# Performance work log

Hardware: AMD Instinct MI355X
Metric: run time of the kernel (lower is better)

Reference implementation:

```python
import jax, jax.numpy as jnp
import numpy as np

NUM_HEADS = 16
N_QUBITS = 8  # both attention d_k and FFN qubit count
LN_EPS = 1e-5


def setup_inputs() -> dict:
    key = jax.random.key(0)
    ks = jax.random.split(key, 8)
    B, S, E, F = 8, 4096, 128, 2048
    return {
        "x": jax.random.normal(ks[0], (B, S, E), dtype=jnp.float32),
        "theta_attn": jax.random.normal(ks[1], (N_QUBITS,), dtype=jnp.float32),
        "phi_ffn": jax.random.normal(ks[2], (N_QUBITS,), dtype=jnp.float32),
        "w1": jax.random.normal(ks[3], (F, N_QUBITS), dtype=jnp.float32) * (1.0 / np.sqrt(N_QUBITS)),
        "b1": jax.random.normal(ks[4], (F,), dtype=jnp.float32) * 0.01,
        "w2": jax.random.normal(ks[5], (E, F), dtype=jnp.float32) * (1.0 / np.sqrt(F)),
        "b2": jax.random.normal(ks[6], (E,), dtype=jnp.float32) * 0.01,
        "gamma1": jnp.ones((E,), dtype=jnp.float32),
        "beta1": jnp.zeros((E,), dtype=jnp.float32),
        "gamma2": jnp.ones((E,), dtype=jnp.float32),
        "beta2": jnp.zeros((E,), dtype=jnp.float32),
    }


def _layernorm(y, g, b):
    m = jnp.mean(y, axis=-1, keepdims=True)
    v = jnp.var(y, axis=-1, keepdims=True)
    return (y - m) * jax.lax.rsqrt(v + LN_EPS) * g + b


def _quantum_attn(x, theta):
    # RX(x_k)RX(theta_k) per wire -> per-wire <Z>=cos(x_k+theta_k); CNOT chain + ring
    # maps Z_j -> Z_0..Z_j (j>=1) and Z_0 -> Z_0..Z_{n-1} (Heisenberg picture),
    # so outputs are cumulative products of cosines within each head.
    B, S, E = x.shape
    a = x.reshape(B, S, NUM_HEADS, N_QUBITS) + theta  # (B,S,H,8)
    cp = jnp.cumprod(jnp.cos(a), axis=-1)
    out = jnp.concatenate([cp[..., -1:], cp[..., 1:]], axis=-1)  # wire0 gets full product
    return out.reshape(B, S, E)


def _quantum_ffn(x, phi):
    # RY(phi_j)RX(x_j)|0> -> <Z_j> = cos(phi_j)*cos(x_j); encoder only reads first N_QUBITS feats
    return jnp.cos(phi) * jnp.cos(x[..., :N_QUBITS])  # (B,S,8)


def reference(x, theta_attn, phi_ffn, w1, b1, w2, b2, gamma1, beta1, gamma2, beta2):
    attn = _quantum_attn(x, theta_attn)
    x1 = _layernorm(x + attn, gamma1, beta1)  # dropout is identity in eval
    q = _quantum_ffn(x1, phi_ffn)
    h = jax.nn.relu(jnp.einsum('bsq,fq->bsf', q, w1) + b1)
    ffn = jnp.einsum('bsf,ef->bse', h, w2) + b2
    return _layernorm(x1 + ffn, gamma2, beta2)
```

## Files before the change

### kernel.cpp

```cpp
#include <hip/hip_runtime.h>
#include <hip/hip_bf16.h>

typedef __attribute__((ext_vector_type(8))) short short8;
typedef __attribute__((ext_vector_type(4))) float f32x4;
typedef __attribute__((ext_vector_type(4))) int int4v;

#define LN_EPS 1e-5f

__device__ __forceinline__ unsigned short bf16rn(float f) {
    unsigned int u = __builtin_bit_cast(unsigned int, f);
    u = u + 0x7fffu + ((u >> 16) & 1u);
    return (unsigned short)(u >> 16);
}

__device__ __forceinline__ unsigned cvt_pk(float lo, float hi) {
    unsigned r;
    asm("v_cvt_pk_bf16_f32 %0, %1, %2" : "=v"(r) : "v"(lo), "v"(hi));
    return r;
}

__global__ __launch_bounds__(256) void k_pre(const float* __restrict__ x,
                                             const float* __restrict__ theta,
                                             const float* __restrict__ phi,
                                             const float* __restrict__ gamma1,
                                             const float* __restrict__ beta1,
                                             const float* __restrict__ w1,
                                             const float* __restrict__ b1,
                                             const float* __restrict__ w2,
                                             float* __restrict__ x1,
                                             unsigned short* __restrict__ qpad,
                                             unsigned short* __restrict__ w2b,
                                             unsigned short* __restrict__ w1p) {
    const int tid = threadIdx.x;
    const int bid = blockIdx.x;

    if (bid >= 2048) {
        const int pid = bid - 2048;
        if (pid < 256) {
            int i = (pid * 256 + tid) * 4;
            float4 v = *(const float4*)(w2 + i);
            ushort4 r;
            r.x = bf16rn(v.x); r.y = bf16rn(v.y); r.z = bf16rn(v.z); r.w = bf16rn(v.w);
            *(ushort4*)(w2b + i) = r;
        } else {
            int f = (pid - 256) * 256 + tid;
            float4 wa = *(const float4*)(w1 + (size_t)f * 8);
            float4 wb = *(const float4*)(w1 + (size_t)f * 8 + 4);
            short8 r0, r1;
            r0[0] = (short)bf16rn(wa.x); r0[1] = (short)bf16rn(wa.y);
            r0[2] = (short)bf16rn(wa.z); r0[3] = (short)bf16rn(wa.w);
            r0[4] = (short)bf16rn(wb.x); r0[5] = (short)bf16rn(wb.y);
            r0[6] = (short)bf16rn(wb.z); r0[7] = (short)bf16rn(wb.w);
            r1 = short8{0, 0, 0, 0, 0, 0, 0, 0};
            r1[0] = (short)bf16rn(b1[f]);
            short8 z = short8{0, 0, 0, 0, 0, 0, 0, 0};
            unsigned short* row = w1p + (size_t)f * 32;
            *(short8*)(row) = r0;
            *(short8*)(row + 8) = r1;
            *(short8*)(row + 16) = z;
            *(short8*)(row + 24) = z;
        }
        return;
    }

    const int g = tid >> 4, li = tid & 15;
    const int tok = bid * 16 + g;

    const float* xr = x + (size_t)tok * 128 + li * 8;
    float4 va = *(const float4*)xr;
    float4 vb = *(const float4*)(xr + 4);
    float v[8] = {va.x, va.y, va.z, va.w, vb.x, vb.y, vb.z, vb.w};

    float c[8];
#pragma unroll
    for (int k = 0; k < 8; ++k) c[k] = __cosf(v[k] + theta[k]);
    float cp[8];
    cp[0] = c[0];
#pragma unroll
    for (int k = 1; k < 8; ++k) cp[k] = cp[k - 1] * c[k];

    float y[8];
    y[0] = v[0] + cp[7];
#pragma unroll
    for (int k = 1; k < 8; ++k) y[k] = v[k] + cp[k];

    float s1 = 0.f, s2 = 0.f;
#pragma unroll
    for (int k = 0; k < 8; ++k) { s1 += y[k]; s2 += y[k] * y[k]; }
#pragma unroll
    for (int m = 1; m < 16; m <<= 1) {
        s1 += __shfl_xor(s1, m);
        s2 += __shfl_xor(s2, m);
    }
    float mean = s1 * (1.f / 128.f);
    float var = s2 * (1.f / 128.f) - mean * mean;
    float rs = rsqrtf(var + LN_EPS);

    float4 ga = *(const float4*)(gamma1 + li * 8);
    float4 gb = *(const float4*)(gamma1 + li * 8 + 4);
    float4 ba = *(const float4*)(beta1 + li * 8);
    float4 bb = *(const float4*)(beta1 + li * 8 + 4);
    float gam[8] = {ga.x, ga.y, ga.z, ga.w, gb.x, gb.y, gb.z, gb.w};
    float bet[8] = {ba.x, ba.y, ba.z, ba.w, bb.x, bb.y, bb.z, bb.w};

    float o[8];
#pragma unroll
    for (int k = 0; k < 8; ++k) o[k] = (y[k] - mean) * rs * gam[k] + bet[k];

    float* x1r = x1 + (size_t)tok * 128 + li * 8;
    *(float4*)x1r = make_float4(o[0], o[1], o[2], o[3]);
    *(float4*)(x1r + 4) = make_float4(o[4], o[5], o[6], o[7]);

    if (li == 0) {
        short8 qr;
#pragma unroll
        for (int k = 0; k < 8; ++k)
            qr[k] = (short)bf16rn(__cosf(phi[k]) * __cosf(o[k]));
        *(short8*)(qpad + (size_t)tok * 32) = qr;
    } else if (li < 4) {
        short8 z = short8{0, 0, 0, 0, 0, 0, 0, 0};
        if (li == 1) z[0] = (short)0x3F80;
        *(short8*)(qpad + (size_t)tok * 32 + li * 8) = z;
    }
}

__global__ __launch_bounds__(512, 4) void k_ffn(const float* __restrict__ x1,
                                                const unsigned short* __restrict__ qpad,
                                                const unsigned short* __restrict__ w2b,
                                                const unsigned short* __restrict__ w1p,
                                                const float* __restrict__ b2,
                                                const float* __restrict__ g2,
                                                const float* __restrict__ be2,
                                                float* __restrict__ out) {
    const int tid = threadIdx.x;
    const int wv = tid >> 6;
    const int kh = wv >> 2;
    const int sub = wv & 3;
    const int nh = sub & 1;
    const int mw = sub >> 1;
    const int lane = tid & 63;
    const int li = lane & 15;
    const int lg = lane >> 4;
    const int Tb = blockIdx.x * 64;
    const int lt0 = mw * 32;
    const int t0 = Tb + lt0;

    __shared__ __align__(16) char smem[65536 + 1024];
    unsigned short* Bs = (unsigned short*)smem;
    float (*red)[132] = (float(*)[132])smem;
    float (*sums)[4] = (float(*)[4])(smem + 65536);

    short8 qf[2];
#pragma unroll
    for (int mt = 0; mt < 2; ++mt)
        qf[mt] = *(const short8*)(qpad + (size_t)(t0 + mt * 16 + li) * 32 + lg * 8);

    const int arow0 = (8 * (li >> 2) + (li & 3)) * 32 + lg * 8;

    f32x4 acc[2][4];
#pragma unroll
    for (int mt = 0; mt < 2; ++mt)
#pragma unroll
        for (int nt = 0; nt < 4; ++nt) acc[mt][nt] = f32x4{0.f, 0.f, 0.f, 0.f};

    const int srow = lane >> 3;
    const int scs = (lane & 7) ^ srow;

    auto stage = [&](int buf, int kb_local) {
        const int kb = kh * 1024 + kb_local;
#pragma unroll
        for (int r = 0; r < 4; ++r) {
            const int e0 = r * 32 + sub * 8;
            const unsigned short* src =
                w2b + (size_t)(e0 + srow) * 2048 + kb + scs * 8;
            unsigned short* dst = Bs + (kh * 2 + buf) * 8192 + e0 * 64;
            __builtin_amdgcn_global_load_lds(
                (const __attribute__((address_space(1))) unsigned int*)src,
                (__attribute__((address_space(3))) unsigned int*)dst,
                16, 0, 0);
        }
    };

    short8 Areg[2][4];
    auto loadA = [&](int kbi_, short8* dst) {
#pragma unroll
        for (int kk = 0; kk < 2; ++kk)
#pragma unroll
            for (int m = 0; m < 2; ++m)
                dst[kk * 2 + m] = *(const short8*)(
                    w1p + (size_t)(kh * 1024 + kbi_ * 64 + kk * 32) * 32 + arow0 + m * 128);
    };

    loadA(0, Areg[0]);
    stage(0, 0);

    const f32x4 zero4 = f32x4{0.f, 0.f, 0.f, 0.f};

#pragma unroll
    for (int kbi = 0; kbi < 16; ++kbi) {
        const int pcur = kbi & 1;
        const int pnext = pcur ^ 1;

        if (kbi < 15) {
            loadA(kbi + 1, Areg[pnext]);
            asm volatile("s_waitcnt vmcnt(4)" ::: "memory");
        } else {
            asm volatile("s_waitcnt vmcnt(0)" ::: "memory");
        }
        __builtin_amdgcn_s_barrier();
        __builtin_amdgcn_sched_barrier(0);
        if (kbi < 15) stage(pnext, (kbi + 1) * 64);

#pragma unroll
        for (int kk = 0; kk < 2; ++kk) {
            short8 A0 = Areg[pcur][kk * 2 + 0];
            short8 A1 = Areg[pcur][kk * 2 + 1];

            const int cs = (kk * 4 + lg) ^ (li & 7);
            const unsigned short* basep =
                Bs + (kh * 2 + pcur) * 8192 + (nh * 64 + li) * 64 + cs * 8;
            short8 bfr[4];
#pragma unroll
            for (int nt = 0; nt < 4; ++nt)
                bfr[nt] = *(const short8*)(basep + nt * 1024);

#pragma unroll
            for (int mt = 0; mt < 2; ++mt) {
                f32x4 p0 = __builtin_amdgcn_mfma_f32_16x16x32_bf16(A0, qf[mt], zero4, 0, 0, 0);
                f32x4 p1 = __builtin_amdgcn_mfma_f32_16x16x32_bf16(A1, qf[mt], zero4, 0, 0, 0);
#pragma unroll
                for (int r = 0; r < 4; ++r) {
                    p0[r] = fmaxf(p0[r], 0.f);
                    p1[r] = fmaxf(p1[r], 0.f);
                }
                int4v ai = {(int)cvt_pk(p0[0], p0[1]), (int)cvt_pk(p0[2], p0[3]),
                            (int)cvt_pk(p1[0], p1[1]), (int)cvt_pk(p1[2], p1[3])};
                short8 a2 = __builtin_bit_cast(short8, ai);
#pragma unroll
                for (int nt = 0; nt < 4; ++nt)
                    acc[mt][nt] = __builtin_amdgcn_mfma_f32_16x16x32_bf16(a2, bfr[nt], acc[mt][nt], 0, 0, 0);
            }
        }
    }
    __syncthreads();

    if (kh == 1) {
#pragma unroll
        for (int mt = 0; mt < 2; ++mt)
#pragma unroll
            for (int nt = 0; nt < 4; ++nt)
#pragma unroll
                for (int r = 0; r < 4; ++r)
                    red[lt0 + mt * 16 + lg * 4 + r][nh * 64 + nt * 16 + li] = acc[mt][nt][r];
    }
    __syncthreads();

    float b2v[4], g2v[4], be2v[4];
    if (kh == 0) {
#pragma unroll
        for (int nt = 0; nt < 4; ++nt) {
            int e = nh * 64 + nt * 16 + li;
            b2v[nt] = b2[e]; g2v[nt] = g2[e]; be2v[nt] = be2[e];
        }
#pragma unroll
        for (int mt = 0; mt < 2; ++mt) {
#pragma unroll
            for (int r = 0; r < 4; ++r) {
                const int ltok = lt0 + mt * 16 + lg * 4 + r;
                const int tok = Tb + ltok;
                const float* x1r = x1 + (size_t)tok * 128 + nh * 64 + li;
                float s1 = 0.f, s2 = 0.f;
#pragma unroll
                for (int nt = 0; nt < 4; ++nt) {
                    float v = acc[mt][nt][r] + red[ltok][nh * 64 + nt * 16 + li] +
                              b2v[nt] + x1r[nt * 16];
                    acc[mt][nt][r] = v;
                    s1 += v; s2 += v * v;
                }
#pragma unroll
                for (int m = 1; m < 16; m <<= 1) {
                    s1 += __shfl_xor(s1, m);
                    s2 += __shfl_xor(s2, m);
                }
                if (li == 0) {
                    sums[ltok][nh * 2 + 0] = s1;
                    sums[ltok][nh * 2 + 1] = s2;
                }
            }
        }
    }
    __syncthreads();

    if (kh == 0) {
#pragma unroll
        for (int mt = 0; mt < 2; ++mt) {
#pragma unroll
            for (int r = 0; r < 4; ++r) {
                const int ltok = lt0 + mt * 16 + lg * 4 + r;
                const int tok = Tb + ltok;
                float s1 = sums[ltok][0] + sums[ltok][2];
                float s2 = sums[ltok][1] + sums[ltok][3];
                float mean = s1 * (1.f / 128.f);
                float var = s2 * (1.f / 128.f) - mean * mean;
                float rs = rsqrtf(var + LN_EPS);
                float* orow = out + (size_t)tok * 128 + nh * 64 + li;
#pragma unroll
                for (int nt = 0; nt < 4; ++nt)
                    orow[nt * 16] = (acc[mt][nt][r] - mean) * rs * g2v[nt] + be2v[nt];
            }
        }
    }
}

extern "C" void kernel_launch(void* const* d_in, const int* in_sizes, int n_in,
                              void* d_out, int out_size, void* d_ws, size_t ws_size,
                              hipStream_t stream) {
    const float* x      = (const float*)d_in[0];
    const float* theta  = (const float*)d_in[1];
    const float* phi    = (const float*)d_in[2];
    const float* w1     = (const float*)d_in[3];
    const float* b1     = (const float*)d_in[4];
    const float* w2     = (const float*)d_in[5];
    const float* b2     = (const float*)d_in[6];
    const float* gamma1 = (const float*)d_in[7];
    const float* beta1  = (const float*)d_in[8];
    const float* gamma2 = (const float*)d_in[9];
    const float* beta2  = (const float*)d_in[10];
    float* out = (float*)d_out;

    char* ws = (char*)d_ws;
    unsigned short* w2b  = (unsigned short*)ws;
    unsigned short* w1p  = (unsigned short*)(ws + (512 << 10));
    unsigned short* qpad = (unsigned short*)(ws + (1 << 20));

    k_pre<<<2312, 256, 0, stream>>>(x, theta, phi, gamma1, beta1, w1, b1, w2,
                                    out, qpad, w2b, w1p);
    k_ffn<<<512, 512, 0, stream>>>(out, qpad, w2b, w1p, b2, gamma2, beta2, out);
}
```

Baseline: 51.04 us.

## Software-pipeline first GEMM one K-block ahead of second GEMM

Restructures the fused FFN loop so the hidden-activation fragments for the next K-block (first small MFMA, ReLU, bf16 pack) are computed after the current block's second-GEMM MFMAs, keeping a double-buffered set of hidden fragments. The aim is to break the dependency between the first and second MFMA within an iteration so the matrix pipe stays busy without waiting on the intermediate conversion. The cost is extra registers for the hidden-fragment buffer, an added wait and a prologue with a full sync.

```diff
diff --git a/kernel.cpp b/kernel.cpp
--- a/kernel.cpp
+++ b/kernel.cpp
@@ -181,53 +181,27 @@
         }
     };
 
-    short8 Areg[2][4];
-    auto loadA = [&](int kbi_, short8* dst) {
+    short8 Areg[4];
+    short8 hfrag[2][2][2];
+
+    auto loadA = [&](int kbi_) {
 #pragma unroll
         for (int kk = 0; kk < 2; ++kk)
 #pragma unroll
             for (int m = 0; m < 2; ++m)
-                dst[kk * 2 + m] = *(const short8*)(
+                Areg[kk * 2 + m] = *(const short8*)(
                     w1p + (size_t)(kh * 1024 + kbi_ * 64 + kk * 32) * 32 + arow0 + m * 128);
     };
 
-    loadA(0, Areg[0]);
-    stage(0, 0);
-
     const f32x4 zero4 = f32x4{0.f, 0.f, 0.f, 0.f};
 
-#pragma unroll
-    for (int kbi = 0; kbi < 16; ++kbi) {
-        const int pcur = kbi & 1;
-        const int pnext = pcur ^ 1;
-
-        if (kbi < 15) {
-            loadA(kbi + 1, Areg[pnext]);
-            asm volatile("s_waitcnt vmcnt(4)" ::: "memory");
-        } else {
-            asm volatile("s_waitcnt vmcnt(0)" ::: "memory");
-        }
-        __builtin_amdgcn_s_barrier();
-        __builtin_amdgcn_sched_barrier(0);
-        if (kbi < 15) stage(pnext, (kbi + 1) * 64);
-
-#pragma unroll
-        for (int kk = 0; kk < 2; ++kk) {
-            short8 A0 = Areg[pcur][kk * 2 + 0];
-            short8 A1 = Areg[pcur][kk * 2 + 1];
-
-            const int cs = (kk * 4 + lg) ^ (li & 7);
-            const unsigned short* basep =
-                Bs + (kh * 2 + pcur) * 8192 + (nh * 64 + li) * 64 + cs * 8;
-            short8 bfr[4];
-#pragma unroll
-            for (int nt = 0; nt < 4; ++nt)
-                bfr[nt] = *(const short8*)(basep + nt * 1024);
-
+    auto gemm1 = [&](int phase) {
+#pragma unroll
+        for (int kk = 0; kk < 2; ++kk)
 #pragma unroll
             for (int mt = 0; mt < 2; ++mt) {
-                f32x4 p0 = __builtin_amdgcn_mfma_f32_16x16x32_bf16(A0, qf[mt], zero4, 0, 0, 0);
-                f32x4 p1 = __builtin_amdgcn_mfma_f32_16x16x32_bf16(A1, qf[mt], zero4, 0, 0, 0);
+                f32x4 p0 = __builtin_amdgcn_mfma_f32_16x16x32_bf16(Areg[kk * 2 + 0], qf[mt], zero4, 0, 0, 0);
+                f32x4 p1 = __builtin_amdgcn_mfma_f32_16x16x32_bf16(Areg[kk * 2 + 1], qf[mt], zero4, 0, 0, 0);
 #pragma unroll
                 for (int r = 0; r < 4; ++r) {
                     p0[r] = fmaxf(p0[r], 0.f);
@@ -235,11 +209,51 @@
                 }
                 int4v ai = {(int)cvt_pk(p0[0], p0[1]), (int)cvt_pk(p0[2], p0[3]),
                             (int)cvt_pk(p1[0], p1[1]), (int)cvt_pk(p1[2], p1[3])};
-                short8 a2 = __builtin_bit_cast(short8, ai);
+                hfrag[phase][kk][mt] = __builtin_bit_cast(short8, ai);
+            }
+    };
+
+    stage(0, 0);
+    loadA(0);
+    asm volatile("s_waitcnt vmcnt(0)" ::: "memory");
+    gemm1(0);
+    __syncthreads();
+
+#pragma unroll
+    for (int kbi = 0; kbi < 16; ++kbi) {
+        const int pcur = kbi & 1;
+        const int pnext = pcur ^ 1;
+
+        if (kbi < 15) {
+            loadA(kbi + 1);
+            asm volatile("s_waitcnt vmcnt(4)" ::: "memory");
+        } else {
+            asm volatile("s_waitcnt vmcnt(0)" ::: "memory");
+        }
+        __builtin_amdgcn_s_barrier();
+        __builtin_amdgcn_sched_barrier(0);
+        if (kbi < 15) stage(pnext, (kbi + 1) * 64);
+
+#pragma unroll
+        for (int kk = 0; kk < 2; ++kk) {
+            const int cs = (kk * 4 + lg) ^ (li & 7);
+            const unsigned short* basep =
+                Bs + (kh * 2 + pcur) * 8192 + (nh * 64 + li) * 64 + cs * 8;
+            short8 bfr[4];
+#pragma unroll
+            for (int nt = 0; nt < 4; ++nt)
+                bfr[nt] = *(const short8*)(basep + nt * 1024);
+#pragma unroll
+            for (int mt = 0; mt < 2; ++mt)
 #pragma unroll
                 for (int nt = 0; nt < 4; ++nt)
-                    acc[mt][nt] = __builtin_amdgcn_mfma_f32_16x16x32_bf16(a2, bfr[nt], acc[mt][nt], 0, 0, 0);
-            }
+                    acc[mt][nt] = __builtin_amdgcn_mfma_f32_16x16x32_bf16(
+                        hfrag[pcur][kk][mt], bfr[nt], acc[mt][nt], 0, 0, 0);
+        }
+
+        if (kbi < 15) {
+            asm volatile("s_waitcnt vmcnt(4)" ::: "memory");
+            gemm1(pnext);
         }
     }
     __syncthreads();
```

Result: faster. 49.37 us (-3.3%).
